# Optimization experiments

Measured on AMD Instinct MI355X. Metric: run time of the kernel, lower is better.

## Reference

```python
import jax, jax.numpy as jnp
import numpy as np
import math

N_EMBD = 1024
N_HEAD = 16
HEAD_DIM = N_EMBD // N_HEAD

def setup_inputs() -> dict:
    key = jax.random.key(0)
    ks = jax.random.split(key, 9)
    B, T, C = 2, 2048, N_EMBD
    s = 1.0 / math.sqrt(C)
    return {
        "x": jax.random.normal(ks[0], (B, T, C), dtype=jnp.float32),
        "Wq": jax.random.normal(ks[1], (C, C), dtype=jnp.float32) * s,
        "bq": jnp.zeros((C,), dtype=jnp.float32),
        "Wk": jax.random.normal(ks[2], (C, C), dtype=jnp.float32) * s,
        "bk": jnp.zeros((C,), dtype=jnp.float32),
        "Wv": jax.random.normal(ks[3], (C, C), dtype=jnp.float32) * s,
        "bv": jnp.zeros((C,), dtype=jnp.float32),
        "Wp": jax.random.normal(ks[4], (C, C), dtype=jnp.float32) * s,
        "bp": jnp.zeros((C,), dtype=jnp.float32),
    }

def reference(x, Wq, bq, Wk, bk, Wv, bv, Wp, bp):
    B, T, C = x.shape
    H, D = N_HEAD, HEAD_DIM
    q = (x @ Wq + bq).reshape(B, T, H, D).transpose(0, 2, 1, 3)  # [B,H,T,D]
    k = (x @ Wk + bk).reshape(B, T, H, D).transpose(0, 2, 1, 3)
    v = (x @ Wv + bv).reshape(B, T, H, D).transpose(0, 2, 1, 3)
    att = jnp.einsum('bhqd,bhkd->bhqk', q, k) / math.sqrt(D)
    causal = jnp.tril(jnp.ones((T, T), dtype=bool))
    att = jnp.where(causal, att, -jnp.inf)
    att = jax.nn.softmax(att, axis=-1)
    att = jnp.nan_to_num(att)
    y = jnp.einsum('bhqk,bhkd->bhqd', att, v)
    y = y.transpose(0, 2, 1, 3).reshape(B, T, C)
    return y @ Wp + bp
```

## Files before the change

kernel.cpp:

```cpp
#include <hip/hip_runtime.h>
#include <hip/hip_bf16.h>
#include <stdint.h>

typedef unsigned short u16;
typedef __attribute__((ext_vector_type(8))) short short8;
typedef __attribute__((ext_vector_type(4))) float f32x4;

static __device__ __forceinline__ u16 f2bf(float f) {
  unsigned u = __builtin_bit_cast(unsigned, f);
  u += 0x7fffu + ((u >> 16) & 1u);
  return (u16)(u >> 16);
}

static __device__ __forceinline__ unsigned cvtpk(float lo, float hi) {
  unsigned r;
  asm("v_cvt_pk_bf16_f32 %0, %1, %2" : "=v"(r) : "v"(lo), "v"(hi));
  return r;
}

static __device__ __forceinline__ void gload16(const u16* g, u16* l) {
  __builtin_amdgcn_global_load_lds(
      (__attribute__((address_space(1))) void*)const_cast<u16*>(g),
      (__attribute__((address_space(3))) void*)l, 16, 0, 0);
}

__global__ __launch_bounds__(256) void prep_kernel(
    const float* __restrict__ x, const float* __restrict__ Wq,
    const float* __restrict__ Wk, const float* __restrict__ Wv,
    const float* __restrict__ Wp, u16* __restrict__ xb, u16* __restrict__ wt) {
  __shared__ float tile[64][65];
  int b = blockIdx.x;
  if (b < 2048) {
    size_t i = (size_t)b * 256 + threadIdx.x;
    const float4* xp = (const float4*)x + i * 2;
    float4 a = xp[0], v = xp[1];
    union { u16 u[8]; int4 q; } r;
    r.u[0] = f2bf(a.x); r.u[1] = f2bf(a.y); r.u[2] = f2bf(a.z); r.u[3] = f2bf(a.w);
    r.u[4] = f2bf(v.x); r.u[5] = f2bf(v.y); r.u[6] = f2bf(v.z); r.u[7] = f2bf(v.w);
    *(int4*)(xb + i * 8) = r.q;
  } else {
    int wb = b - 2048;
    int wz = wb >> 8, r8 = wb & 255;
    const float* W = (wz == 0) ? Wq : (wz == 1) ? Wk : (wz == 2) ? Wv : Wp;
    int n0 = (r8 & 15) * 64, k0 = (r8 >> 4) * 64;
    int tx = threadIdx.x & 63, ty = threadIdx.x >> 6;
#pragma unroll
    for (int r = 0; r < 16; ++r)
      tile[ty + 4 * r][tx] = W[(size_t)(k0 + ty + 4 * r) * 1024 + n0 + tx];
    __syncthreads();
    u16* dst = wt + (size_t)wz * 1024 * 1024;
#pragma unroll
    for (int r = 0; r < 16; ++r) {
      int n = ty + 4 * r;
      dst[(size_t)(n0 + n) * 1024 + k0 + tx] = f2bf(tile[tx][n]);
    }
  }
}

template <int EPI, int DBUF>
__global__ __launch_bounds__(256, 2) void gemm128_kernel(
    const u16* __restrict__ A, const u16* __restrict__ Bt, int Kdim,
    int GM, int GN, int RM, int RN,
    u16* __restrict__ qd, u16* __restrict__ kd, u16* __restrict__ vd,
    const float* __restrict__ bq, const float* __restrict__ bk,
    const float* __restrict__ bv, float* __restrict__ outf,
    const float* __restrict__ bias1) {
  __shared__ u16 Alds[(DBUF ? 2 : 1) * 8192];
  __shared__ u16 Blds[(DBUF ? 2 : 1) * 8192];
  int tid = threadIdx.x;
  int lane = tid & 63, w = tid >> 6;
  int l15 = lane & 15, lg = lane >> 4;
  int flat = blockIdx.x;
  int xcd = flat & 7, idx = flat >> 3;
  int rnc = GN / RN;
  int rm = (xcd / rnc) * RM, rn = (xcd % rnc) * RN;
  int im = idx % RM, in_ = idx / RM;
  int m0 = (rm + im) * 128, n0 = (rn + in_) * 128;
  int wm = (w >> 1) * 64, wn = (w & 1) * 64;
  int srow = lane >> 3;
  int colsw = ((lane & 7) * 8) ^ ((srow & 7) * 8);

  const u16* pA[4];
  const u16* pB[4];
  int dls[4];
#pragma unroll
  for (int j = 0; j < 4; ++j) {
    int issue = w * 4 + j;
    int row = issue * 8 + srow;
    pA[j] = A + (size_t)(m0 + row) * Kdim + colsw;
    pB[j] = Bt + (size_t)(n0 + row) * Kdim + colsw;
    dls[j] = issue * 512;
  }
  int kx = (l15 & 7) << 4;
  int ofs0 = (lg * 16) ^ kx, ofs1 = (64 + lg * 16) ^ kx;
  int rbA = (wm + l15) * 128, rbB = (wn + l15) * 128;

  auto stage = [&](int buf) {
    u16* Ad = Alds + buf * 8192;
    u16* Bd = Blds + buf * 8192;
#pragma unroll
    for (int j = 0; j < 4; ++j) {
      gload16(pA[j], Ad + dls[j]);
      gload16(pB[j], Bd + dls[j]);
      pA[j] += 64; pB[j] += 64;
    }
  };

  f32x4 acc[4][4] = {};
  int cur = 0;
  if (DBUF) stage(0);
  for (int kt = 0; kt < Kdim; kt += 64) {
    if (DBUF) {
      __syncthreads();
      if (kt + 64 < Kdim) stage(cur ^ 1);
    } else {
      stage(0);
      __syncthreads();
    }
    const char* Al = (const char*)Alds + cur * 16384;
    const char* Bl = (const char*)Blds + cur * 16384;
    __builtin_amdgcn_s_setprio(1);
#pragma unroll
    for (int kk = 0; kk < 2; ++kk) {
      int o_ = kk ? ofs1 : ofs0;
      short8 a[4], b[4];
#pragma unroll
      for (int mt = 0; mt < 4; ++mt)
        a[mt] = *(const short8*)(Al + (rbA + o_) + mt * 2048);
#pragma unroll
      for (int nt = 0; nt < 4; ++nt)
        b[nt] = *(const short8*)(Bl + (rbB + o_) + nt * 2048);
#pragma unroll
      for (int mt = 0; mt < 4; ++mt)
#pragma unroll
        for (int nt = 0; nt < 4; ++nt)
          acc[mt][nt] = __builtin_amdgcn_mfma_f32_16x16x32_bf16(a[mt], b[nt],
                                                                acc[mt][nt], 0, 0, 0);
    }
    __builtin_amdgcn_s_setprio(0);
    if (!DBUF) __syncthreads();
    cur ^= DBUF;
  }
  if (EPI == 0) {
#pragma unroll
    for (int nt = 0; nt < 4; ++nt) {
      int n = n0 + wn + nt * 16 + l15;
      int wi = n >> 10, nn = n & 1023, h = nn >> 6, d = nn & 63;
      const float* bb = (wi == 0) ? bq : (wi == 1) ? bk : bv;
      float bval = bb[nn];
      if (wi == 2) {
#pragma unroll
        for (int mt = 0; mt < 4; ++mt) {
          int m = m0 + wm + mt * 16 + lg * 4;
          int mb = m >> 11, t = m & 2047;
          unsigned lo = cvtpk(acc[mt][nt][0] + bval, acc[mt][nt][1] + bval);
          unsigned hi = cvtpk(acc[mt][nt][2] + bval, acc[mt][nt][3] + bval);
          *(uint2*)&vd[((size_t)(mb * 16 + h) * 64 + d) * 2048 + t] =
              make_uint2(lo, hi);
        }
      } else {
        u16* dst = (wi == 0) ? qd : kd;
#pragma unroll
        for (int mt = 0; mt < 4; ++mt) {
#pragma unroll
          for (int i = 0; i < 4; ++i) {
            int m = m0 + wm + mt * 16 + lg * 4 + i;
            int mb = m >> 11, t = m & 2047;
            dst[((size_t)(mb * 16 + h) * 2048 + t) * 64 + d] =
                f2bf(acc[mt][nt][i] + bval);
          }
        }
      }
    }
  } else {
#pragma unroll
    for (int nt = 0; nt < 4; ++nt) {
      int n = n0 + wn + nt * 16 + l15;
      float bval = bias1[n];
#pragma unroll
      for (int mt = 0; mt < 4; ++mt) {
#pragma unroll
        for (int i = 0; i < 4; ++i) {
          int m = m0 + wm + mt * 16 + lg * 4 + i;
          outf[(size_t)m * 1024 + n] = acc[mt][nt][i] + bval;
        }
      }
    }
  }
}

__global__ __launch_bounds__(256, 4) void fattn_kernel(const u16* __restrict__ qb,
                                                       const u16* __restrict__ kb,
                                                       const u16* __restrict__ vt,
                                                       u16* __restrict__ y) {
  __shared__ u16 Klds[2 * 4096];
  __shared__ u16 Vlds[2 * 4096];
  __shared__ u16 Plds[4 * 1024];
  int tid = threadIdx.x, lane = tid & 63, w = tid >> 6;
  int l15 = lane & 15, lg = lane >> 4;
  int flat = blockIdx.x;
  int bh = flat & 31;
  int qt = 31 - (flat >> 5);
  size_t base = (size_t)bh * 2048 * 64;
  int mb = bh >> 4, h = bh & 15;
  const float SC = 0.125f * 1.44269504088896340736f;
  const float NINF = -__builtin_inff();

  int r0 = tid >> 3, c0 = ((tid & 7) * 8) ^ ((r0 & 7) << 3);
  int r1 = (256 + tid) >> 3, c1 = ((tid & 7) * 8) ^ ((r1 & 7) << 3);
  const u16* pK0 = kb + base + (size_t)r0 * 64 + c0;
  const u16* pK1 = kb + base + (size_t)r1 * 64 + c1;
  const u16* pV0 = vt + base + (size_t)r0 * 2048 + c0;
  const u16* pV1 = vt + base + (size_t)r1 * 2048 + c1;
  int dk0 = w * 512, dk1 = (256 + w * 64) * 8;
  int kx = (l15 & 7) << 4;
  int rb0 = l15 * 128 + ((lg * 16) ^ kx);
  int rb1 = l15 * 128 + ((64 + lg * 16) ^ kx);
  char* pbase = (char*)Plds + w * 2048;
  int pw0 = l15 * 128 + ((lg * 8) ^ kx);
  int pw1 = l15 * 128 + ((32 + lg * 8) ^ kx);
  int pw2 = l15 * 128 + ((64 + lg * 8) ^ kx);
  int pw3 = l15 * 128 + ((96 + lg * 8) ^ kx);

  int qw = qt * 64 + w * 16;
  int qr = qw + l15;
  short8 qf[2];
#pragma unroll
  for (int kk = 0; kk < 2; ++kk)
    qf[kk] = *(const short8*)&qb[base + (size_t)qr * 64 + kk * 32 + lg * 8];
  f32x4 o[4] = {};
  float mrow = NINF, lrow = 0.f;
  {
    gload16(pK0, Klds + dk0); gload16(pK1, Klds + dk1);
    gload16(pV0, Vlds + dk0); gload16(pV1, Vlds + dk1);
    pK0 += 4096; pK1 += 4096; pV0 += 64; pV1 += 64;
  }
  int cb = 0;
  int ntiles = qt + 1;
  for (int j = 0; j < ntiles; ++j) {
    __syncthreads();
    if (j + 1 < ntiles) {
      u16* kd_ = Klds + (cb ^ 1) * 4096;
      u16* vd_ = Vlds + (cb ^ 1) * 4096;
      gload16(pK0, kd_ + dk0); gload16(pK1, kd_ + dk1);
      gload16(pV0, vd_ + dk0); gload16(pV1, vd_ + dk1);
      pK0 += 4096; pK1 += 4096; pV0 += 64; pV1 += 64;
    }
    const char* kl = (const char*)Klds + cb * 8192;
    const char* vl = (const char*)Vlds + cb * 8192;
    f32x4 s[4] = {};
    __builtin_amdgcn_s_setprio(1);
#pragma unroll
    for (int kk = 0; kk < 2; ++kk) {
      int o_ = kk ? rb1 : rb0;
      short8 ka[4];
#pragma unroll
      for (int nt = 0; nt < 4; ++nt)
        ka[nt] = *(const short8*)(kl + o_ + nt * 2048);
#pragma unroll
      for (int nt = 0; nt < 4; ++nt)
        s[nt] = __builtin_amdgcn_mfma_f32_16x16x32_bf16(ka[nt], qf[kk], s[nt], 0, 0, 0);
    }
    __builtin_amdgcn_s_setprio(0);
    float rs[16];
    if (j == qt) {
      int k0 = j * 64;
#pragma unroll
      for (int nt = 0; nt < 4; ++nt)
#pragma unroll
        for (int i = 0; i < 4; ++i) {
          int ka_ = k0 + nt * 16 + lg * 4 + i;
          rs[nt * 4 + i] = (ka_ > qr) ? NINF : s[nt][i];
        }
    } else {
#pragma unroll
      for (int nt = 0; nt < 4; ++nt)
#pragma unroll
        for (int i = 0; i < 4; ++i) rs[nt * 4 + i] = s[nt][i];
    }
    float rmax = fmaxf(
        fmaxf(fmaxf(fmaxf(rs[0], rs[1]), fmaxf(rs[2], rs[3])),
              fmaxf(fmaxf(rs[4], rs[5]), fmaxf(rs[6], rs[7]))),
        fmaxf(fmaxf(fmaxf(rs[8], rs[9]), fmaxf(rs[10], rs[11])),
              fmaxf(fmaxf(rs[12], rs[13]), fmaxf(rs[14], rs[15]))));
    float tmax = rmax * SC;
    if (!__all(tmax <= mrow + 8.f)) {
      float t2 = fmaxf(tmax, __shfl_xor(tmax, 16));
      t2 = fmaxf(t2, __shfl_xor(t2, 32));
      float vmax = fmaxf(t2, mrow);
      float scale = exp2f(mrow - vmax);
      mrow = vmax;
      lrow *= scale;
#pragma unroll
      for (int dn = 0; dn < 4; ++dn) o[dn] *= scale;
    }
    float p[16];
#pragma unroll
    for (int u = 0; u < 16; ++u) p[u] = exp2f(fmaf(rs[u], SC, -mrow));
    float pr0 = ((p[0] + p[1]) + (p[2] + p[3])) + ((p[4] + p[5]) + (p[6] + p[7]));
    float pr1 = ((p[8] + p[9]) + (p[10] + p[11])) + ((p[12] + p[13]) + (p[14] + p[15]));
    lrow += pr0 + pr1;
    *(uint2*)(pbase + pw0) = make_uint2(cvtpk(p[0], p[1]), cvtpk(p[2], p[3]));
    *(uint2*)(pbase + pw1) = make_uint2(cvtpk(p[4], p[5]), cvtpk(p[6], p[7]));
    *(uint2*)(pbase + pw2) = make_uint2(cvtpk(p[8], p[9]), cvtpk(p[10], p[11]));
    *(uint2*)(pbase + pw3) = make_uint2(cvtpk(p[12], p[13]), cvtpk(p[14], p[15]));
    __builtin_amdgcn_s_setprio(1);
#pragma unroll
    for (int kk = 0; kk < 2; ++kk) {
      int o_ = kk ? rb1 : rb0;
      short8 ap = *(const short8*)(pbase + o_);
#pragma unroll
      for (int dn = 0; dn < 4; ++dn) {
        short8 bv_ = *(const short8*)(vl + o_ + dn * 2048);
        o[dn] = __builtin_amdgcn_mfma_f32_16x16x32_bf16(bv_, ap, o[dn], 0, 0, 0);
      }
    }
    __builtin_amdgcn_s_setprio(0);
    cb ^= 1;
  }
  lrow += __shfl_xor(lrow, 16);
  lrow += __shfl_xor(lrow, 32);
  float inv = 1.f / lrow;
  size_t rb = ((size_t)(mb * 2048 + qr)) * 1024 + (size_t)h * 64;
#pragma unroll
  for (int dn = 0; dn < 4; ++dn) {
    unsigned lo = cvtpk(o[dn][0] * inv, o[dn][1] * inv);
    unsigned hi = cvtpk(o[dn][2] * inv, o[dn][3] * inv);
    *(uint2*)&y[rb + dn * 16 + lg * 4] = make_uint2(lo, hi);
  }
}

extern "C" void kernel_launch(void* const* d_in, const int* in_sizes, int n_in,
                              void* d_out, int out_size, void* d_ws, size_t ws_size,
                              hipStream_t stream) {
  const float* x  = (const float*)d_in[0];
  const float* Wq = (const float*)d_in[1];
  const float* bq = (const float*)d_in[2];
  const float* Wk = (const float*)d_in[3];
  const float* bk = (const float*)d_in[4];
  const float* Wv = (const float*)d_in[5];
  const float* bv = (const float*)d_in[6];
  const float* Wp = (const float*)d_in[7];
  const float* bp = (const float*)d_in[8];
  float* out = (float*)d_out;
  char* ws = (char*)d_ws;
  u16* xb   = (u16*)(ws);
  u16* wt   = (u16*)(ws + ((size_t)8 << 20));
  u16* qbuf = (u16*)(ws + ((size_t)16 << 20));
  u16* kbuf = (u16*)(ws + ((size_t)24 << 20));
  u16* vtb  = (u16*)(ws + ((size_t)32 << 20));
  u16* ybuf = (u16*)(ws + ((size_t)40 << 20));

  prep_kernel<<<dim3(3072), dim3(256), 0, stream>>>(x, Wq, Wk, Wv, Wp, xb, wt);
  gemm128_kernel<0, 0><<<dim3(768), dim3(256), 0, stream>>>(
      xb, wt, 1024, 32, 24, 8, 12,
      qbuf, kbuf, vtb, bq, bk, bv, (float*)nullptr, (const float*)nullptr);
  fattn_kernel<<<dim3(1024), dim3(256), 0, stream>>>(qbuf, kbuf, vtb, ybuf);
  gemm128_kernel<1, 1><<<dim3(256), dim3(256), 0, stream>>>(
      ybuf, wt + (size_t)3 * 1024 * 1024, 1024, 32, 8, 8, 4,
      (u16*)nullptr, (u16*)nullptr, (u16*)nullptr,
      (const float*)nullptr, (const float*)nullptr, (const float*)nullptr, out, bp);
  (void)in_sizes; (void)n_in; (void)out_size; (void)ws_size;
}
```

Baseline: 106.3 us.

## Split long causal attention tiles across KV halves and merge with combine kernel

Query tiles in the upper half of the sequence are split into two blocks, each covering half of the KV range, writing unnormalized partial outputs plus running max and sum. A new combine kernel merges the two partials with log-sum-exp rescaling into the final y. This bounds per-block work to 16 tiles to improve load balance and tail behavior on the GPU. It costs an extra launch, extra global traffic for partials, and bf16 rounding of unnormalized partials.

New measurement: 109.8 us. +3.3%, slower.

```diff
diff --git a/kernel.cpp b/kernel.cpp
--- a/kernel.cpp
+++ b/kernel.cpp
@@ -10,6 +10,11 @@
   unsigned u = __builtin_bit_cast(unsigned, f);
   u += 0x7fffu + ((u >> 16) & 1u);
   return (u16)(u >> 16);
+}
+
+static __device__ __forceinline__ float bf2f(u16 v) {
+  unsigned u = (unsigned)v << 16;
+  return __builtin_bit_cast(float, u);
 }
 
 static __device__ __forceinline__ unsigned cvtpk(float lo, float hi) {
@@ -189,10 +194,11 @@
   }
 }
 
-__global__ __launch_bounds__(256, 4) void fattn_kernel(const u16* __restrict__ qb,
-                                                       const u16* __restrict__ kb,
-                                                       const u16* __restrict__ vt,
-                                                       u16* __restrict__ y) {
+__global__ __launch_bounds__(256, 4) void fattn_kernel(
+    const u16* __restrict__ qb, const u16* __restrict__ kb,
+    const u16* __restrict__ vt, u16* __restrict__ y,
+    u16* __restrict__ poA, u16* __restrict__ poB,
+    float2* __restrict__ mlA, float2* __restrict__ mlB) {
   __shared__ u16 Klds[2 * 4096];
   __shared__ u16 Vlds[2 * 4096];
   __shared__ u16 Plds[4 * 1024];
@@ -200,7 +206,15 @@
   int l15 = lane & 15, lg = lane >> 4;
   int flat = blockIdx.x;
   int bh = flat & 31;
-  int qt = 31 - (flat >> 5);
+  int seg = flat >> 5;
+  int qt, j0, j1, mode;
+  if (seg < 16) {
+    qt = 16 + seg; j0 = 0; j1 = 16; mode = 1;
+  } else {
+    int k = (seg - 16) >> 1;
+    if ((seg & 1) == 0) { qt = 31 - k; j0 = 16; j1 = qt + 1; mode = 2; }
+    else               { qt = 15 - k; j0 = 0;  j1 = qt + 1; mode = 0; }
+  }
   size_t base = (size_t)bh * 2048 * 64;
   int mb = bh >> 4, h = bh & 15;
   const float SC = 0.125f * 1.44269504088896340736f;
@@ -208,10 +222,10 @@
 
   int r0 = tid >> 3, c0 = ((tid & 7) * 8) ^ ((r0 & 7) << 3);
   int r1 = (256 + tid) >> 3, c1 = ((tid & 7) * 8) ^ ((r1 & 7) << 3);
-  const u16* pK0 = kb + base + (size_t)r0 * 64 + c0;
-  const u16* pK1 = kb + base + (size_t)r1 * 64 + c1;
-  const u16* pV0 = vt + base + (size_t)r0 * 2048 + c0;
-  const u16* pV1 = vt + base + (size_t)r1 * 2048 + c1;
+  const u16* pK0 = kb + base + (size_t)(j0 * 64 + r0) * 64 + c0;
+  const u16* pK1 = kb + base + (size_t)(j0 * 64 + r1) * 64 + c1;
+  const u16* pV0 = vt + base + (size_t)r0 * 2048 + j0 * 64 + c0;
+  const u16* pV1 = vt + base + (size_t)r1 * 2048 + j0 * 64 + c1;
   int dk0 = w * 512, dk1 = (256 + w * 64) * 8;
   int kx = (l15 & 7) << 4;
   int rb0 = l15 * 128 + ((lg * 16) ^ kx);
@@ -236,10 +250,9 @@
     pK0 += 4096; pK1 += 4096; pV0 += 64; pV1 += 64;
   }
   int cb = 0;
-  int ntiles = qt + 1;
-  for (int j = 0; j < ntiles; ++j) {
+  for (int j = j0; j < j1; ++j) {
     __syncthreads();
-    if (j + 1 < ntiles) {
+    if (j + 1 < j1) {
       u16* kd_ = Klds + (cb ^ 1) * 4096;
       u16* vd_ = Vlds + (cb ^ 1) * 4096;
       gload16(pK0, kd_ + dk0); gload16(pK1, kd_ + dk1);
@@ -320,14 +333,47 @@
   }
   lrow += __shfl_xor(lrow, 16);
   lrow += __shfl_xor(lrow, 32);
-  float inv = 1.f / lrow;
-  size_t rb = ((size_t)(mb * 2048 + qr)) * 1024 + (size_t)h * 64;
-#pragma unroll
-  for (int dn = 0; dn < 4; ++dn) {
-    unsigned lo = cvtpk(o[dn][0] * inv, o[dn][1] * inv);
-    unsigned hi = cvtpk(o[dn][2] * inv, o[dn][3] * inv);
-    *(uint2*)&y[rb + dn * 16 + lg * 4] = make_uint2(lo, hi);
-  }
+  if (mode == 0) {
+    float inv = 1.f / lrow;
+    size_t rb = ((size_t)(mb * 2048 + qr)) * 1024 + (size_t)h * 64;
+#pragma unroll
+    for (int dn = 0; dn < 4; ++dn) {
+      unsigned lo = cvtpk(o[dn][0] * inv, o[dn][1] * inv);
+      unsigned hi = cvtpk(o[dn][2] * inv, o[dn][3] * inv);
+      *(uint2*)&y[rb + dn * 16 + lg * 4] = make_uint2(lo, hi);
+    }
+  } else {
+    int prow = bh * 1024 + (qr - 1024);
+    u16* pdst = (mode == 1 ? poA : poB) + (size_t)prow * 64;
+#pragma unroll
+    for (int dn = 0; dn < 4; ++dn) {
+      unsigned lo = cvtpk(o[dn][0], o[dn][1]);
+      unsigned hi = cvtpk(o[dn][2], o[dn][3]);
+      *(uint2*)&pdst[dn * 16 + lg * 4] = make_uint2(lo, hi);
+    }
+    if (lg == 0) {
+      float2* ml = (mode == 1 ? mlA : mlB);
+      ml[prow] = make_float2(mrow, lrow);
+    }
+  }
+}
+
+__global__ __launch_bounds__(256) void combine_kernel(
+    const u16* __restrict__ poA, const u16* __restrict__ poB,
+    const float2* __restrict__ mlA, const float2* __restrict__ mlB,
+    u16* __restrict__ y) {
+  int idx = blockIdx.x * 256 + threadIdx.x;
+  int row = idx >> 6, d = idx & 63;
+  float2 a = mlA[row], b = mlB[row];
+  float m = fmaxf(a.x, b.x);
+  float ea = exp2f(a.x - m), eb = exp2f(b.x - m);
+  float l = a.y * ea + b.y * eb;
+  float oa = bf2f(poA[(size_t)row * 64 + d]);
+  float ob = bf2f(poB[(size_t)row * 64 + d]);
+  float yv = (oa * ea + ob * eb) / l;
+  int bh = row >> 10, qr = 1024 + (row & 1023);
+  int mb = bh >> 4, h = bh & 15;
+  y[((size_t)(mb * 2048 + qr)) * 1024 + h * 64 + d] = f2bf(yv);
 }
 
 extern "C" void kernel_launch(void* const* d_in, const int* in_sizes, int n_in,
@@ -350,12 +396,18 @@
   u16* kbuf = (u16*)(ws + ((size_t)24 << 20));
   u16* vtb  = (u16*)(ws + ((size_t)32 << 20));
   u16* ybuf = (u16*)(ws + ((size_t)40 << 20));
+  u16*    poA = (u16*)(ws);
+  u16*    poB = (u16*)(ws + ((size_t)5 << 20));
+  float2* mlA = (float2*)(ws + ((size_t)13 << 20));
+  float2* mlB = (float2*)(ws + ((size_t)13 << 20) + (512 << 10));
 
   prep_kernel<<<dim3(3072), dim3(256), 0, stream>>>(x, Wq, Wk, Wv, Wp, xb, wt);
   gemm128_kernel<0, 0><<<dim3(768), dim3(256), 0, stream>>>(
       xb, wt, 1024, 32, 24, 8, 12,
       qbuf, kbuf, vtb, bq, bk, bv, (float*)nullptr, (const float*)nullptr);
-  fattn_kernel<<<dim3(1024), dim3(256), 0, stream>>>(qbuf, kbuf, vtb, ybuf);
+  fattn_kernel<<<dim3(1536), dim3(256), 0, stream>>>(qbuf, kbuf, vtb, ybuf,
+                                                     poA, poB, mlA, mlB);
+  combine_kernel<<<dim3(8192), dim3(256), 0, stream>>>(poA, poB, mlA, mlB, ybuf);
   gemm128_kernel<1, 1><<<dim3(256), dim3(256), 0, stream>>>(
       ybuf, wt + (size_t)3 * 1024 * 1024, 1024, 32, 8, 8, 4,
       (u16*)nullptr, (u16*)nullptr, (u16*)nullptr,
```
